# Optimization experiments

Measured on AMD Instinct MI355X. Metric: run time of the kernel, lower is better.

The kernel has to match this reference:

```python
import jax, jax.numpy as jnp
import numpy as np

D_IN = 1024
D_OUT = 1024
N_HEADS = 16
HEAD_DIM = D_OUT // N_HEADS


def setup_inputs() -> dict:
    key = jax.random.key(0)
    ks = jax.random.split(key, 6)
    s = 0.02
    x = jax.random.normal(ks[0], (2, 2048, D_IN), dtype=jnp.float32)
    Wq = jax.random.normal(ks[1], (D_IN, D_OUT), dtype=jnp.float32) * s
    Wk = jax.random.normal(ks[2], (D_IN, D_OUT), dtype=jnp.float32) * s
    Wv = jax.random.normal(ks[3], (D_IN, D_OUT), dtype=jnp.float32) * s
    Wo = jax.random.normal(ks[4], (D_OUT, D_OUT), dtype=jnp.float32) * s
    bo = jax.random.normal(ks[5], (D_OUT,), dtype=jnp.float32) * s
    return {"x": x, "Wq": Wq, "Wk": Wk, "Wv": Wv, "Wo": Wo, "bo": bo}


def reference(x, Wq, Wk, Wv, Wo, bo):
    B, S, _ = x.shape
    # project and split heads: (B, H, S, Dh)
    def split(t):
        return t.reshape(B, S, N_HEADS, HEAD_DIM).transpose(0, 2, 1, 3)
    q = split(x @ Wq)
    k = split(x @ Wk)
    v = split(x @ Wv)
    scores = jnp.einsum('bhqd,bhkd->bhqk', q, k)  # (B,H,S,S)
    causal = jnp.tril(jnp.ones((S, S), dtype=bool))
    scores = jnp.where(causal, scores, -jnp.inf)
    attn = jax.nn.softmax(scores / np.sqrt(HEAD_DIM).astype(np.float32), axis=-1)
    ctx = jnp.einsum('bhqk,bhkd->bhqd', attn, v)
    ctx = ctx.transpose(0, 2, 1, 3).reshape(B, S, D_OUT)
    return ctx @ Wo + bo
```

## Files before the change

kernel.cpp:

```cpp
#include <hip/hip_runtime.h>
#include <hip/hip_bf16.h>
#include <math.h>

typedef __attribute__((ext_vector_type(8))) short bf16x8;
typedef __attribute__((ext_vector_type(8))) unsigned short u16x8;
typedef __attribute__((ext_vector_type(4))) float f32x4;

__device__ __forceinline__ unsigned short f2bf(float f) {
  union { float f; unsigned u; } c; c.f = f;
  unsigned u = c.u;
  u += 0x7fffu + ((u >> 16) & 1u);
  return (unsigned short)(u >> 16);
}
__device__ __forceinline__ unsigned fb(float x) {
  union { float f; unsigned u; } c; c.f = x; return c.u;
}
__device__ __forceinline__ void async16(const unsigned short* g, unsigned short* l) {
  __builtin_amdgcn_global_load_lds(
      (const __attribute__((address_space(1))) unsigned int*)g,
      (__attribute__((address_space(3))) unsigned int*)l, 16, 0, 0);
}

__global__ __launch_bounds__(256) void prep_kernel(
    const float* __restrict__ x, const float* __restrict__ Wq,
    const float* __restrict__ Wk, const float* __restrict__ Wv,
    const float* __restrict__ Wo, unsigned short* __restrict__ Xb,
    unsigned short* __restrict__ Wqkvt, unsigned short* __restrict__ Wot) {
  const int z = blockIdx.z;
  if (z == 4) {
    const int bid = blockIdx.y * 32 + blockIdx.x;
#pragma unroll
    for (int i = 0; i < 4; ++i) {
      const int idx = (bid * 4 + i) * 256 + threadIdx.x;
      float4 v = ((const float4*)x)[idx];
      ushort4 o;
      o.x = f2bf(v.x); o.y = f2bf(v.y); o.z = f2bf(v.z); o.w = f2bf(v.w);
      ((ushort4*)Xb)[idx] = o;
    }
    return;
  }
  __shared__ float t[32][33];
  const float* src = (z == 0) ? Wq : (z == 1) ? Wk : (z == 2) ? Wv : Wo;
  unsigned short* dst = (z < 3) ? (Wqkvt + (size_t)z * 1024 * 1024) : Wot;
  const float scale = (z == 0) ? 0.18033688f : 1.0f;
  int tx = threadIdx.x & 31, ty = threadIdx.x >> 5;
  int bx = blockIdx.x, by = blockIdx.y;
#pragma unroll
  for (int i = 0; i < 4; ++i)
    t[ty + i * 8][tx] = src[(size_t)(by * 32 + ty + i * 8) * 1024 + bx * 32 + tx];
  __syncthreads();
#pragma unroll
  for (int i = 0; i < 4; ++i)
    dst[(size_t)(bx * 32 + ty + i * 8) * 1024 + by * 32 + tx] = f2bf(t[tx][ty + i * 8] * scale);
}

__global__ __launch_bounds__(256) void gemm_qkv(
    const unsigned short* __restrict__ A, const unsigned short* __restrict__ Bt,
    unsigned short* __restrict__ Qh, unsigned short* __restrict__ Kh,
    unsigned short* __restrict__ Vt, int K) {
  __shared__ unsigned short As [128][32];
  __shared__ unsigned short As2[128][32];
  __shared__ unsigned short Bs [128][32];
  __shared__ unsigned short Bs2[128][32];
  const int flat = blockIdx.x;
  const int xcd = flat & 7, idx = flat >> 3;
  const int mg = xcd >> 1, ng = xcd & 1;
  const int m0 = (mg * 8 + (idx & 7)) * 128;
  const int n0 = (ng * 12 + (idx >> 3)) * 128;
  const int tid = threadIdx.x;
  const int wave = tid >> 6, lane = tid & 63;
  const int quad = lane >> 4, l16 = lane & 15;
  const int wm = (wave >> 1) * 64, wn = (wave & 1) * 64;
  const int srow = tid >> 2, sch = (tid & 3) * 8;
  f32x4 acc[4][4] = {};

  for (int k0 = 0; k0 < K; k0 += 64) {
    __syncthreads();
    async16(A  + (size_t)(m0 + srow) * K + k0 + sch,           &As [srow][sch]);
    async16(A  + (size_t)(m0 + srow + 64) * K + k0 + sch,      &As [srow + 64][sch]);
    async16(A  + (size_t)(m0 + srow) * K + k0 + 32 + sch,      &As2[srow][sch]);
    async16(A  + (size_t)(m0 + srow + 64) * K + k0 + 32 + sch, &As2[srow + 64][sch]);
    async16(Bt + (size_t)(n0 + srow) * K + k0 + sch,           &Bs [srow][sch]);
    async16(Bt + (size_t)(n0 + srow + 64) * K + k0 + sch,      &Bs [srow + 64][sch]);
    async16(Bt + (size_t)(n0 + srow) * K + k0 + 32 + sch,      &Bs2[srow][sch]);
    async16(Bt + (size_t)(n0 + srow + 64) * K + k0 + 32 + sch, &Bs2[srow + 64][sch]);
    __syncthreads();
    bf16x8 af[4], bfr[4];
#pragma unroll
    for (int i = 0; i < 4; ++i) {
      af[i]  = *(const bf16x8*)&As[wm + i * 16 + l16][quad * 8];
      bfr[i] = *(const bf16x8*)&Bs[wn + i * 16 + l16][quad * 8];
    }
#pragma unroll
    for (int mi = 0; mi < 4; ++mi)
#pragma unroll
      for (int ni = 0; ni < 4; ++ni)
        acc[mi][ni] = __builtin_amdgcn_mfma_f32_16x16x32_bf16(af[mi], bfr[ni], acc[mi][ni], 0, 0, 0);
#pragma unroll
    for (int i = 0; i < 4; ++i) {
      af[i]  = *(const bf16x8*)&As2[wm + i * 16 + l16][quad * 8];
      bfr[i] = *(const bf16x8*)&Bs2[wn + i * 16 + l16][quad * 8];
    }
#pragma unroll
    for (int mi = 0; mi < 4; ++mi)
#pragma unroll
      for (int ni = 0; ni < 4; ++ni)
        acc[mi][ni] = __builtin_amdgcn_mfma_f32_16x16x32_bf16(af[mi], bfr[ni], acc[mi][ni], 0, 0, 0);
  }

#pragma unroll
  for (int mi = 0; mi < 4; ++mi) {
#pragma unroll
    for (int ni = 0; ni < 4; ++ni) {
      const int col = n0 + wn + ni * 16 + l16;
      const int token0 = m0 + wm + mi * 16 + quad * 4;
      const int bb = token0 >> 11, s0 = token0 & 2047;
      if (col < 2048) {
        const int hh = (col & 1023) >> 6, d = col & 63;
        unsigned short* dst = (col < 1024) ? Qh : Kh;
        dst += ((size_t)(bb * 16 + hh) * 2048 + s0) * 64 + d;
#pragma unroll
        for (int r = 0; r < 4; ++r) dst[(size_t)r * 64] = f2bf(acc[mi][ni][r]);
      } else {
        const int vc = col - 2048, hh = vc >> 6, d = vc & 63;
        ushort4 us;
        us.x = f2bf(acc[mi][ni][0]); us.y = f2bf(acc[mi][ni][1]);
        us.z = f2bf(acc[mi][ni][2]); us.w = f2bf(acc[mi][ni][3]);
        *(ushort4*)&Vt[(((size_t)(bb * 16 + hh) * 64 + (s0 >> 5)) * 64 + d) * 32 + (s0 & 31)] = us;
      }
    }
  }
}

__global__ __launch_bounds__(256) void gemm_out(
    const unsigned short* __restrict__ A, const unsigned short* __restrict__ Bt,
    float* __restrict__ C, const float* __restrict__ bias, int N, int K) {
  __shared__ unsigned short As [128][32];
  __shared__ unsigned short As2[128][32];
  __shared__ unsigned short Bs [64][32];
  __shared__ unsigned short Bs2[64][32];
  const int flat = blockIdx.x;
  const int xcd = flat & 7, idx = flat >> 3;
  const int mg = xcd >> 1, ng = xcd & 1;
  const int m0 = (mg * 8 + (idx & 7)) * 128;
  const int n0 = (ng * 8 + (idx >> 3)) * 64;
  const int tid = threadIdx.x;
  const int wave = tid >> 6, lane = tid & 63;
  const int quad = lane >> 4, l16 = lane & 15;
  const int wm = (wave >> 1) * 64, wn = (wave & 1) * 32;
  const int srow = tid >> 2, sch = (tid & 3) * 8;
  f32x4 acc[4][2] = {};

  for (int k0 = 0; k0 < K; k0 += 64) {
    __syncthreads();
    async16(A  + (size_t)(m0 + srow) * K + k0 + sch,           &As [srow][sch]);
    async16(A  + (size_t)(m0 + srow + 64) * K + k0 + sch,      &As [srow + 64][sch]);
    async16(A  + (size_t)(m0 + srow) * K + k0 + 32 + sch,      &As2[srow][sch]);
    async16(A  + (size_t)(m0 + srow + 64) * K + k0 + 32 + sch, &As2[srow + 64][sch]);
    async16(Bt + (size_t)(n0 + srow) * K + k0 + sch,           &Bs [srow][sch]);
    async16(Bt + (size_t)(n0 + srow) * K + k0 + 32 + sch,      &Bs2[srow][sch]);
    __syncthreads();
    bf16x8 af[4], bfr[2];
#pragma unroll
    for (int i = 0; i < 4; ++i)
      af[i] = *(const bf16x8*)&As[wm + i * 16 + l16][quad * 8];
#pragma unroll
    for (int i = 0; i < 2; ++i)
      bfr[i] = *(const bf16x8*)&Bs[wn + i * 16 + l16][quad * 8];
#pragma unroll
    for (int mi = 0; mi < 4; ++mi)
#pragma unroll
      for (int ni = 0; ni < 2; ++ni)
        acc[mi][ni] = __builtin_amdgcn_mfma_f32_16x16x32_bf16(af[mi], bfr[ni], acc[mi][ni], 0, 0, 0);
#pragma unroll
    for (int i = 0; i < 4; ++i)
      af[i] = *(const bf16x8*)&As2[wm + i * 16 + l16][quad * 8];
#pragma unroll
    for (int i = 0; i < 2; ++i)
      bfr[i] = *(const bf16x8*)&Bs2[wn + i * 16 + l16][quad * 8];
#pragma unroll
    for (int mi = 0; mi < 4; ++mi)
#pragma unroll
      for (int ni = 0; ni < 2; ++ni)
        acc[mi][ni] = __builtin_amdgcn_mfma_f32_16x16x32_bf16(af[mi], bfr[ni], acc[mi][ni], 0, 0, 0);
  }
#pragma unroll
  for (int mi = 0; mi < 4; ++mi)
#pragma unroll
    for (int ni = 0; ni < 2; ++ni) {
      const int col = n0 + wn + ni * 16 + l16;
      const float bv = bias[col];
      const int row0 = m0 + wm + mi * 16 + quad * 4;
#pragma unroll
      for (int r = 0; r < 4; ++r)
        C[(size_t)(row0 + r) * N + col] = acc[mi][ni][r] + bv;
    }
}

__global__ __launch_bounds__(256, 3) void attn_kernel(
    const unsigned short* __restrict__ Qh, const unsigned short* __restrict__ Kh,
    const unsigned short* __restrict__ Vt, unsigned short* __restrict__ ctx) {
  const int id = blockIdx.x;
  const int j = id >> 3;
  const int bh = (id & 7) | ((j & 3) << 3);
  const int s = 63 - (j >> 2);
  const int b = bh >> 4, h = bh & 15;
  const int wave = threadIdx.x >> 6, lane = threadIdx.x & 63;
  const int quad = lane >> 4, l16 = lane & 15;
  const int q0 = s * 32;
  const int T = (s + 2) >> 1;
  const int lo = (T * wave) >> 2;
  const int hi = (T * (wave + 1)) >> 2;

  __shared__ __align__(16) char smem[20480];
  unsigned short (*Pt)[32][72] = (unsigned short (*)[32][72])smem;

  const unsigned short* Qp = Qh + (size_t)bh * 2048 * 64;
  const unsigned short* Kg = Kh + (size_t)bh * 2048 * 64;
  const unsigned short* Vg = Vt + (size_t)bh * 64 * 2048;

  bf16x8 qf[2][2];
#pragma unroll
  for (int qg = 0; qg < 2; ++qg)
#pragma unroll
    for (int kk = 0; kk < 2; ++kk)
      qf[qg][kk] = *(const bf16x8*)(Qp + (size_t)(q0 + qg * 16 + l16) * 64 + kk * 32 + quad * 8);

  bf16x8 ones;
#pragma unroll
  for (int jj = 0; jj < 8; ++jj) ones[jj] = (short)0x3F80;

  f32x4 o[5][2] = {};

  for (int jt = lo; jt < hi; ++jt) {
    const int k0 = jt * 64;
    f32x4 st[4][2] = {};
#pragma unroll
    for (int keyg = 0; keyg < 4; ++keyg) {
#pragma unroll
      for (int kk = 0; kk < 2; ++kk) {
        bf16x8 kf = *(const bf16x8*)(Kg + (size_t)(k0 + keyg * 16 + l16) * 64 + kk * 32 + quad * 8);
#pragma unroll
        for (int qg = 0; qg < 2; ++qg)
          st[keyg][qg] = __builtin_amdgcn_mfma_f32_16x16x32_bf16(kf, qf[qg][kk], st[keyg][qg], 0, 0, 0);
      }
    }
    bf16x8 vf[4][2];
#pragma unroll
    for (int dg = 0; dg < 4; ++dg)
#pragma unroll
      for (int half = 0; half < 2; ++half)
        vf[dg][half] = *(const bf16x8*)(Vg + (size_t)(2 * jt + half) * 2048 + (dg * 16 + l16) * 32 + quad * 8);
    if (jt == T - 1) {
#pragma unroll
      for (int keyg = 0; keyg < 4; ++keyg)
#pragma unroll
        for (int r = 0; r < 4; ++r) {
          const int key = k0 + keyg * 16 + quad * 4 + r;
#pragma unroll
          for (int qg = 0; qg < 2; ++qg)
            if (key > q0 + qg * 16 + l16) st[keyg][qg][r] = -INFINITY;
        }
    }
#pragma unroll
    for (int qg = 0; qg < 2; ++qg) {
#pragma unroll
      for (int keyg = 0; keyg < 4; ++keyg) {
        float p0 = exp2f(st[keyg][qg][0]);
        float p1 = exp2f(st[keyg][qg][1]);
        float p2 = exp2f(st[keyg][qg][2]);
        float p3 = exp2f(st[keyg][qg][3]);
        uint2 pk;
        pk.x = __builtin_amdgcn_perm(fb(p1), fb(p0), 0x07060302u);
        pk.y = __builtin_amdgcn_perm(fb(p3), fb(p2), 0x07060302u);
        *(uint2*)&Pt[wave][qg * 16 + l16][keyg * 16 + quad * 4] = pk;
      }
    }
    bf16x8 pb[2][2];
#pragma unroll
    for (int qg = 0; qg < 2; ++qg)
#pragma unroll
      for (int half = 0; half < 2; ++half)
        pb[qg][half] = *(const bf16x8*)&Pt[wave][qg * 16 + l16][half * 32 + quad * 8];
#pragma unroll
    for (int dg = 0; dg < 4; ++dg)
#pragma unroll
      for (int qg = 0; qg < 2; ++qg) {
        o[dg][qg] = __builtin_amdgcn_mfma_f32_16x16x32_bf16(vf[dg][0], pb[qg][0], o[dg][qg], 0, 0, 0);
        o[dg][qg] = __builtin_amdgcn_mfma_f32_16x16x32_bf16(vf[dg][1], pb[qg][1], o[dg][qg], 0, 0, 0);
      }
#pragma unroll
    for (int qg = 0; qg < 2; ++qg) {
      o[4][qg] = __builtin_amdgcn_mfma_f32_16x16x32_bf16(ones, pb[qg][0], o[4][qg], 0, 0, 0);
      o[4][qg] = __builtin_amdgcn_mfma_f32_16x16x32_bf16(ones, pb[qg][1], o[4][qg], 0, 0, 0);
    }
  }

  float (*Os0)[2][64][4] = (float (*)[2][64][4])(smem);
  float (*Os1)[2][64][4] = (float (*)[2][64][4])(smem + 10240);

  __syncthreads();
  if (wave == 1 || wave == 3) {
    float (*Os)[2][64][4] = (wave == 1) ? Os0 : Os1;
#pragma unroll
    for (int qg = 0; qg < 2; ++qg)
#pragma unroll
      for (int dg = 0; dg < 5; ++dg)
        *(f32x4*)&Os[dg][qg][lane][0] = o[dg][qg];
  }
  __syncthreads();
  if (wave == 0 || wave == 2) {
    float (*Os)[2][64][4] = (wave == 0) ? Os0 : Os1;
#pragma unroll
    for (int qg = 0; qg < 2; ++qg)
#pragma unroll
      for (int dg = 0; dg < 5; ++dg) {
        f32x4 o1 = *(const f32x4*)&Os[dg][qg][lane][0];
#pragma unroll
        for (int r = 0; r < 4; ++r) o[dg][qg][r] += o1[r];
      }
  }
  __syncthreads();
  if (wave == 2) {
#pragma unroll
    for (int qg = 0; qg < 2; ++qg)
#pragma unroll
      for (int dg = 0; dg < 5; ++dg)
        *(f32x4*)&Os0[dg][qg][lane][0] = o[dg][qg];
  }
  __syncthreads();
  if (wave == 0) {
#pragma unroll
    for (int qg = 0; qg < 2; ++qg) {
#pragma unroll
      for (int dg = 0; dg < 5; ++dg) {
        f32x4 o1 = *(const f32x4*)&Os0[dg][qg][lane][0];
#pragma unroll
        for (int r = 0; r < 4; ++r) o[dg][qg][r] += o1[r];
      }
      const float inv = 1.f / o[4][qg][0];
      const size_t base = (size_t)(b * 2048 + q0 + qg * 16 + l16) * 1024 + h * 64;
#pragma unroll
      for (int dg = 0; dg < 4; ++dg) {
        ushort4 us;
        us.x = f2bf(o[dg][qg][0] * inv); us.y = f2bf(o[dg][qg][1] * inv);
        us.z = f2bf(o[dg][qg][2] * inv); us.w = f2bf(o[dg][qg][3] * inv);
        *(ushort4*)&ctx[base + dg * 16 + quad * 4] = us;
      }
    }
  }
}

extern "C" void kernel_launch(void* const* d_in, const int* in_sizes, int n_in,
                              void* d_out, int out_size, void* d_ws, size_t ws_size,
                              hipStream_t stream) {
  const float* x  = (const float*)d_in[0];
  const float* Wq = (const float*)d_in[1];
  const float* Wk = (const float*)d_in[2];
  const float* Wv = (const float*)d_in[3];
  const float* Wo = (const float*)d_in[4];
  const float* bo = (const float*)d_in[5];
  float* out = (float*)d_out;

  char* ws = (char*)d_ws;
  unsigned short* Xb    = (unsigned short*)(ws);
  unsigned short* Wqkvt = (unsigned short*)(ws + (size_t)8  * 1048576);
  unsigned short* Wot   = (unsigned short*)(ws + (size_t)14 * 1048576);
  unsigned short* Qhb   = (unsigned short*)(ws + (size_t)16 * 1048576);
  unsigned short* Khb   = (unsigned short*)(ws + (size_t)24 * 1048576);
  unsigned short* Vtb   = (unsigned short*)(ws + (size_t)32 * 1048576);
  unsigned short* CT    = (unsigned short*)(ws + (size_t)40 * 1048576);

  prep_kernel<<<dim3(32, 32, 5), 256, 0, stream>>>(x, Wq, Wk, Wv, Wo, Xb, Wqkvt, Wot);
  gemm_qkv<<<768, 256, 0, stream>>>(Xb, Wqkvt, Qhb, Khb, Vtb, 1024);
  attn_kernel<<<2048, 256, 0, stream>>>(Qhb, Khb, Vtb, CT);
  gemm_out<<<512, 256, 0, stream>>>(CT, Wot, out, bo, 1024, 1024);
}
```

Measured before the change: 185.4 us.

## Feed P to PV MFMA directly from registers using 16x16x16 bf16 ops

Replaces the LDS round-trip for the probability tile (write P to shared memory, read it back transposed) with the 16x16x16 bf16 MFMA, whose B-operand layout matches the QK^T accumulator layout. This removes the LDS stores and loads per key tile. In exchange it issues twice as many smaller MFMAs with lower throughput per instruction, and reads V as 8-byte loads instead of 16-byte loads. The V indexing assumes a matching transposed layout from the prep kernel.

```diff
diff --git a/kernel.cpp b/kernel.cpp
--- a/kernel.cpp
+++ b/kernel.cpp
@@ -3,8 +3,14 @@
 #include <math.h>
 
 typedef __attribute__((ext_vector_type(8))) short bf16x8;
-typedef __attribute__((ext_vector_type(8))) unsigned short u16x8;
+typedef __attribute__((ext_vector_type(4))) short bf16x4;
 typedef __attribute__((ext_vector_type(4))) float f32x4;
+
+#if __has_builtin(__builtin_amdgcn_mfma_f32_16x16x16_bf16)
+#define MFMA16K16(a, b, c) __builtin_amdgcn_mfma_f32_16x16x16_bf16(a, b, c, 0, 0, 0)
+#else
+#define MFMA16K16(a, b, c) __builtin_amdgcn_mfma_f32_16x16x16bf16_1k(a, b, c, 0, 0, 0)
+#endif
 
 __device__ __forceinline__ unsigned short f2bf(float f) {
   union { float f; unsigned u; } c; c.f = f;
@@ -213,7 +219,6 @@
   const int hi = (T * (wave + 1)) >> 2;
 
   __shared__ __align__(16) char smem[20480];
-  unsigned short (*Pt)[32][72] = (unsigned short (*)[32][72])smem;
 
   const unsigned short* Qp = Qh + (size_t)bh * 2048 * 64;
   const unsigned short* Kg = Kh + (size_t)bh * 2048 * 64;
@@ -226,9 +231,9 @@
     for (int kk = 0; kk < 2; ++kk)
       qf[qg][kk] = *(const bf16x8*)(Qp + (size_t)(q0 + qg * 16 + l16) * 64 + kk * 32 + quad * 8);
 
-  bf16x8 ones;
-#pragma unroll
-  for (int jj = 0; jj < 8; ++jj) ones[jj] = (short)0x3F80;
+  bf16x4 ones4;
+#pragma unroll
+  for (int jj = 0; jj < 4; ++jj) ones4[jj] = (short)0x3F80;
 
   f32x4 o[5][2] = {};
 
@@ -245,12 +250,15 @@
           st[keyg][qg] = __builtin_amdgcn_mfma_f32_16x16x32_bf16(kf, qf[qg][kk], st[keyg][qg], 0, 0, 0);
       }
     }
-    bf16x8 vf[4][2];
+    bf16x4 vf[4][4];
 #pragma unroll
     for (int dg = 0; dg < 4; ++dg)
 #pragma unroll
-      for (int half = 0; half < 2; ++half)
-        vf[dg][half] = *(const bf16x8*)(Vg + (size_t)(2 * jt + half) * 2048 + (dg * 16 + l16) * 32 + quad * 8);
+      for (int keyg = 0; keyg < 4; ++keyg) {
+        const int t  = 2 * jt + (keyg >> 1);
+        const int s5 = (keyg & 1) * 16 + quad * 4;
+        vf[dg][keyg] = *(const bf16x4*)(Vg + ((size_t)t * 64 + dg * 16 + l16) * 32 + s5);
+      }
     if (jt == T - 1) {
 #pragma unroll
       for (int keyg = 0; keyg < 4; ++keyg)
@@ -270,29 +278,14 @@
         float p1 = exp2f(st[keyg][qg][1]);
         float p2 = exp2f(st[keyg][qg][2]);
         float p3 = exp2f(st[keyg][qg][3]);
-        uint2 pk;
-        pk.x = __builtin_amdgcn_perm(fb(p1), fb(p0), 0x07060302u);
-        pk.y = __builtin_amdgcn_perm(fb(p3), fb(p2), 0x07060302u);
-        *(uint2*)&Pt[wave][qg * 16 + l16][keyg * 16 + quad * 4] = pk;
-      }
-    }
-    bf16x8 pb[2][2];
-#pragma unroll
-    for (int qg = 0; qg < 2; ++qg)
-#pragma unroll
-      for (int half = 0; half < 2; ++half)
-        pb[qg][half] = *(const bf16x8*)&Pt[wave][qg * 16 + l16][half * 32 + quad * 8];
-#pragma unroll
-    for (int dg = 0; dg < 4; ++dg)
-#pragma unroll
-      for (int qg = 0; qg < 2; ++qg) {
-        o[dg][qg] = __builtin_amdgcn_mfma_f32_16x16x32_bf16(vf[dg][0], pb[qg][0], o[dg][qg], 0, 0, 0);
-        o[dg][qg] = __builtin_amdgcn_mfma_f32_16x16x32_bf16(vf[dg][1], pb[qg][1], o[dg][qg], 0, 0, 0);
-      }
-#pragma unroll
-    for (int qg = 0; qg < 2; ++qg) {
-      o[4][qg] = __builtin_amdgcn_mfma_f32_16x16x32_bf16(ones, pb[qg][0], o[4][qg], 0, 0, 0);
-      o[4][qg] = __builtin_amdgcn_mfma_f32_16x16x32_bf16(ones, pb[qg][1], o[4][qg], 0, 0, 0);
+        union { uint2 u; bf16x4 h; } pk;
+        pk.u.x = __builtin_amdgcn_perm(fb(p1), fb(p0), 0x07060302u);
+        pk.u.y = __builtin_amdgcn_perm(fb(p3), fb(p2), 0x07060302u);
+#pragma unroll
+        for (int dg = 0; dg < 4; ++dg)
+          o[dg][qg] = MFMA16K16(vf[dg][keyg], pk.h, o[dg][qg]);
+        o[4][qg] = MFMA16K16(ones4, pk.h, o[4][qg]);
+      }
     }
   }
 
```

Result: slower. 199.4 us (+7.6%).
